# Kernel tuning notes

Measured on AMD Instinct MI355X. Metric: run time of the kernel, lower is better.

Reference implementation:

```python
import jax, jax.numpy as jnp
import numpy as np

B, T, D, H, F = 4, 2048, 1024, 16, 4096
HD = D // H
EPS = 1e-5


def setup_inputs() -> dict:
    key = jax.random.key(0)
    ks = jax.random.split(key, 10)
    s = lambda fan_in: 1.0 / np.sqrt(fan_in)
    return {
        "x": jax.random.normal(ks[0], (B, T, D), jnp.float32),
        "ln1_g": jnp.ones((D,), jnp.float32),
        "ln1_b": jnp.zeros((D,), jnp.float32),
        "ln2_g": jnp.ones((D,), jnp.float32),
        "ln2_b": jnp.zeros((D,), jnp.float32),
        "Wq": jax.random.normal(ks[1], (H, D, HD), jnp.float32) * s(D),
        "Wk": jax.random.normal(ks[2], (H, D, HD), jnp.float32) * s(D),
        "Wv": jax.random.normal(ks[3], (H, D, HD), jnp.float32) * s(D),
        "Wo": jax.random.normal(ks[4], (D, D), jnp.float32) * s(D),
        "bo": jnp.zeros((D,), jnp.float32),
        "W1": jax.random.normal(ks[5], (D, F), jnp.float32) * s(D),
        "b1": jnp.zeros((F,), jnp.float32),
        "W2": jax.random.normal(ks[6], (F, D), jnp.float32) * s(F),
        "b2": jnp.zeros((D,), jnp.float32),
    }


def _layernorm(x, g, b):
    mu = jnp.mean(x, axis=-1, keepdims=True)
    var = jnp.mean(jnp.square(x - mu), axis=-1, keepdims=True)
    return (x - mu) * jax.lax.rsqrt(var + EPS) * g + b


def reference(x, ln1_g, ln1_b, ln2_g, ln2_b, Wq, Wk, Wv, Wo, bo, W1, b1, W2, b2):
    Bc, Tc, Dc = x.shape
    xn = _layernorm(x, ln1_g, ln1_b)
    # per-head projections (source loops over heads; here batched over h)
    q = jnp.einsum('btd,hdk->bhtk', xn, Wq)
    k = jnp.einsum('btd,hdk->bhtk', xn, Wk)
    v = jnp.einsum('btd,hdk->bhtk', xn, Wv)
    scale = jnp.asarray(Dc, x.dtype) ** -0.5  # C**-0.5 with C = embedding_dim
    scores = jnp.einsum('bhtk,bhsk->bhts', q, k) * scale
    causal = jnp.tril(jnp.ones((Tc, Tc), bool))
    scores = jnp.where(causal, scores, -jnp.inf)
    attn = jax.nn.softmax(scores, axis=-1)
    out = jnp.einsum('bhts,bhsk->bhtk', attn, v)
    out = out.transpose(0, 2, 1, 3).reshape(Bc, Tc, Dc)  # concat heads
    attn_out = out @ Wo + bo
    h = attn_out + x  # residual 1
    hn = _layernorm(h, ln2_g, ln2_b)
    ff = jax.nn.relu(hn @ W1 + b1) @ W2 + b2
    return ff + h  # residual 2
```

## Files before the change

### kernel.cpp

```cpp
#include <hip/hip_runtime.h>
#include <hip/hip_bf16.h>

#define NB 4
#define NT 2048
#define ND 1024
#define NH 16
#define NHD 64
#define NF 4096
#define MTOK (NB*NT)

typedef float f32x4 __attribute__((ext_vector_type(4)));
typedef __bf16 bf16x8 __attribute__((ext_vector_type(8)));
typedef short s16x8 __attribute__((ext_vector_type(8)));
typedef unsigned short ushort_t;

__device__ inline ushort_t f2bf(float f) {
    unsigned int u = __builtin_bit_cast(unsigned int, f);
    unsigned int r = (u + 0x7FFFu + ((u >> 16) & 1u)) >> 16;
    return (ushort_t)r;
}

__device__ __forceinline__ void async_load16(const void* g, void* l) {
    __builtin_amdgcn_global_load_lds(
        (const __attribute__((address_space(1))) void*)g,
        (__attribute__((address_space(3))) void*)l, 16, 0, 0);
}

__device__ __forceinline__ unsigned int cvt_pk_bf16(float lo, float hi) {
    unsigned int r;
    asm("v_cvt_pk_bf16_f32 %0, %1, %2" : "=v"(r) : "v"(lo), "v"(hi));
    return r;
}

__device__ __forceinline__ float exp2_fast(float x) {
    float r;
    asm("v_exp_f32 %0, %1" : "=v"(r) : "v"(x));
    return r;
}

__global__ __launch_bounds__(256)
void transpose_to_bf16(const float* __restrict__ src, ushort_t* __restrict__ dst,
                       int R, int C) {
    __shared__ float tile[32][33];
    int c0 = blockIdx.x * 32, r0 = blockIdx.y * 32;
    #pragma unroll
    for (int i = 0; i < 32; i += 8)
        tile[threadIdx.y + i][threadIdx.x] =
            src[(size_t)(r0 + threadIdx.y + i) * C + c0 + threadIdx.x];
    __syncthreads();
    #pragma unroll
    for (int i = 0; i < 32; i += 8)
        dst[(size_t)(c0 + threadIdx.y + i) * R + r0 + threadIdx.x] =
            f2bf(tile[threadIdx.x][threadIdx.y + i]);
}

__global__ __launch_bounds__(256)
void transpose_qkv_to_bf16(const float* __restrict__ Wq, const float* __restrict__ Wk,
                           const float* __restrict__ Wv, ushort_t* __restrict__ dst) {
    __shared__ float tile[32][33];
    int z = blockIdx.z;
    int w = z >> 4, h = z & 15;
    const float* src = (w == 0 ? Wq : (w == 1 ? Wk : Wv)) + (size_t)h * ND * NHD;
    const float sc = (w == 0) ? 0.03125f * 1.44269504f : 1.0f;
    ushort_t* out = dst + ((size_t)w * ND + h * NHD) * ND;
    int c0 = blockIdx.x * 32, r0 = blockIdx.y * 32;
    #pragma unroll
    for (int i = 0; i < 32; i += 8)
        tile[threadIdx.y + i][threadIdx.x] =
            src[(size_t)(r0 + threadIdx.y + i) * NHD + c0 + threadIdx.x];
    __syncthreads();
    #pragma unroll
    for (int i = 0; i < 32; i += 8)
        out[(size_t)(c0 + threadIdx.y + i) * ND + r0 + threadIdx.x] =
            f2bf(tile[threadIdx.x][threadIdx.y + i] * sc);
}

__global__ __launch_bounds__(256)
void layernorm_to_bf16(const float* __restrict__ x, const float* __restrict__ g,
                       const float* __restrict__ bvec, ushort_t* __restrict__ out) {
    int row = blockIdx.x;
    const float4* xr = (const float4*)(x + (size_t)row * ND);
    float4 v = xr[threadIdx.x];
    float s = v.x + v.y + v.z + v.w;
    float s2 = v.x * v.x + v.y * v.y + v.z * v.z + v.w * v.w;
    #pragma unroll
    for (int o = 32; o >= 1; o >>= 1) {
        s += __shfl_xor(s, o);
        s2 += __shfl_xor(s2, o);
    }
    __shared__ float red[8];
    int wave = threadIdx.x >> 6, lane = threadIdx.x & 63;
    if (lane == 0) { red[wave] = s; red[4 + wave] = s2; }
    __syncthreads();
    float ts = red[0] + red[1] + red[2] + red[3];
    float ts2 = red[4] + red[5] + red[6] + red[7];
    float mu = ts * (1.f / ND);
    float var = ts2 * (1.f / ND) - mu * mu;
    float rs = rsqrtf(var + 1e-5f);
    float4 gv = ((const float4*)g)[threadIdx.x];
    float4 bv = ((const float4*)bvec)[threadIdx.x];
    ushort4 o4;
    o4.x = f2bf((v.x - mu) * rs * gv.x + bv.x);
    o4.y = f2bf((v.y - mu) * rs * gv.y + bv.y);
    o4.z = f2bf((v.z - mu) * rs * gv.z + bv.z);
    o4.w = f2bf((v.w - mu) * rs * gv.w + bv.w);
    ((ushort4*)(out + (size_t)row * ND))[threadIdx.x] = o4;
}

template<int BN, bool HAS_BIAS, bool RELU, bool HAS_RES, bool OUT_F32>
__global__ __launch_bounds__(512, 2)
void gemm256(const ushort_t* __restrict__ A, const ushort_t* __restrict__ Bt,
             const float* __restrict__ bias, const float* __restrict__ res,
             void* __restrict__ outp, int M, int N, int K) {
    constexpr int NFR = BN / 64;
    constexpr int BISS = BN / 64;
    __shared__ __align__(16) ushort_t As[2][256 * 64];
    __shared__ __align__(16) ushort_t Bs[2][BN * 64];
    const int t = threadIdx.x;
    const int wave = t >> 6, lane = t & 63;
    const int wm = wave >> 2, wn = wave & 3;
    const int g = lane >> 4, l16 = lane & 15;
    int wid = blockIdx.y * gridDim.x + blockIdx.x;
    const int cpx = (gridDim.x * gridDim.y) >> 3;
    wid = (wid & 7) * cpx + (wid >> 3);
    const int m0 = (wid / gridDim.x) * 256;
    const int n0 = (wid % gridDim.x) * BN;
    const int lrow8 = lane >> 3;
    const int srcCol = ((lane & 7) ^ lrow8) * 8;
    const ushort_t* Abase = A + (size_t)m0 * K + srcCol;
    const ushort_t* Bbase = Bt + (size_t)n0 * K + srcCol;
    const int NKT = K >> 6;

    f32x4 acc[8][NFR] = {};

    auto stageA = [&](int kt, int slot) {
        #pragma unroll
        for (int j = 0; j < 4; j++) {
            const int rowbase = j * 64 + wave * 8;
            async_load16(Abase + (size_t)(rowbase + lrow8) * K + kt * 64,
                         &As[slot][rowbase * 64]);
        }
    };
    auto stageB = [&](int kt, int slot) {
        #pragma unroll
        for (int j = 0; j < BISS; j++) {
            const int rowbase = j * 64 + wave * 8;
            async_load16(Bbase + (size_t)(rowbase + lrow8) * K + kt * 64,
                         &Bs[slot][rowbase * 64]);
        }
    };

    stageA(0, 0);
    stageB(0, 0);
    stageB(1, 1);

    for (int kt = 0; kt < NKT; ++kt) {
        const int cur = kt & 1;
        if (kt == NKT - 1) {
            asm volatile("s_waitcnt vmcnt(0)" ::: "memory");
        } else if constexpr (BN == 256) {
            asm volatile("s_waitcnt vmcnt(4)" ::: "memory");
        } else {
            asm volatile("s_waitcnt vmcnt(2)" ::: "memory");
        }
        __builtin_amdgcn_s_barrier();

        const ushort_t* as = As[cur];
        const ushort_t* bs = Bs[cur];

        bf16x8 bfr[NFR][2];
        #pragma unroll
        for (int nf = 0; nf < NFR; nf++)
            #pragma unroll
            for (int ks = 0; ks < 2; ks++) {
                const int row = wn * (BN / 4) + nf * 16 + l16;
                int a = row * 128 + ks * 64 + 16 * g;
                a ^= (row & 7) << 4;
                bfr[nf][ks] = *(const bf16x8*)((const char*)bs + a);
            }
        if (kt + 1 < NKT) stageA(kt + 1, cur ^ 1);

        #pragma unroll
        for (int q = 0; q < 4; q++) {
            if (q == 2) {
                __builtin_amdgcn_s_barrier();
                if (kt + 2 < NKT) stageB(kt + 2, cur);
            }
            bf16x8 af[2][2];
            #pragma unroll
            for (int mi2 = 0; mi2 < 2; mi2++)
                #pragma unroll
                for (int ks = 0; ks < 2; ks++) {
                    const int row = wm * 128 + (q * 2 + mi2) * 16 + l16;
                    int a = row * 128 + ks * 64 + 16 * g;
                    a ^= (row & 7) << 4;
                    af[mi2][ks] = *(const bf16x8*)((const char*)as + a);
                }
            __builtin_amdgcn_s_setprio(1);
            #pragma unroll
            for (int mi2 = 0; mi2 < 2; mi2++)
                #pragma unroll
                for (int nf = 0; nf < NFR; nf++)
                    #pragma unroll
                    for (int ks = 0; ks < 2; ks++)
                        acc[q * 2 + mi2][nf] = __builtin_amdgcn_mfma_f32_16x16x32_bf16(
                            af[mi2][ks], bfr[nf][ks], acc[q * 2 + mi2][nf], 0, 0, 0);
            __builtin_amdgcn_s_setprio(0);
        }
    }

    const int gr0 = m0 + wm * 128 + g * 4;
    const int gc0 = n0 + wn * (BN / 4) + l16;
    #pragma unroll
    for (int mi = 0; mi < 8; mi++) {
        #pragma unroll
        for (int nf = 0; nf < NFR; nf++) {
            const int col = gc0 + nf * 16;
            float bb = 0.f;
            if constexpr (HAS_BIAS) bb = bias[col];
            #pragma unroll
            for (int r = 0; r < 4; r++) {
                const int row = gr0 + mi * 16 + r;
                float v = acc[mi][nf][r] + bb;
                if constexpr (RELU) v = fmaxf(v, 0.f);
                if constexpr (HAS_RES) v += res[(size_t)row * N + col];
                if constexpr (OUT_F32)
                    ((float*)outp)[(size_t)row * N + col] = v;
                else
                    ((ushort_t*)outp)[(size_t)row * N + col] = f2bf(v);
            }
        }
    }
}

__global__ __launch_bounds__(256)
void attn_kernel(const ushort_t* __restrict__ qkv, ushort_t* __restrict__ out) {
    __shared__ __align__(16) ushort_t Ks[2][64 * 64];
    __shared__ __align__(16) ushort_t Vt[2][64 * 64];
    __shared__ unsigned int Pw[4][32][35];
    const int L = blockIdx.y * gridDim.x + blockIdx.x;
    const int xcd = L & 7, kk = L >> 3;
    const int bh = ((kk & 7) << 3) | xcd;
    const int pairIdx = kk >> 3;
    const int b = bh >> 4, h = bh & 15;
    const int t = threadIdx.x, wave = t >> 6, lane = t & 63;
    const int g = lane >> 4, q16 = lane & 15;
    const size_t base = ((size_t)b * NT) * 3072 + h * NHD;
    const ushort_t* qp_base = qkv + base;
    const ushort_t* kb = qkv + base + 1024;
    const ushort_t* vb = qkv + base + 2048;
    const int krw = lane >> 3, kck = lane & 7;
    const int ksrc = (kck ^ krw) * 8;
    const int vkp = t >> 3, vdg = t & 7;

    bf16x8 ones_f;
    {
        uint4 u = {0x3F803F80u, 0x3F803F80u, 0x3F803F80u, 0x3F803F80u};
        ones_f = __builtin_bit_cast(bf16x8, u);
    }

    auto stageK = [&](int kv, int buf) {
        #pragma unroll
        for (int c = 0; c < 2; c++) {
            const int rowbase = c * 32 + wave * 8;
            async_load16(kb + (size_t)(kv * 64 + rowbase + krw) * 3072 + ksrc,
                         &Ks[buf][rowbase * 64]);
        }
    };
    auto loadV = [&](int kv, s16x8& v0, s16x8& v1) {
        const ushort_t* vp = vb + (size_t)(kv * 64 + 2 * vkp) * 3072 + vdg * 8;
        v0 = *(const s16x8*)vp;
        v1 = *(const s16x8*)(vp + 3072);
    };
    auto writeV = [&](int buf, const s16x8& v0, const s16x8& v1) {
        const uint4 w0 = __builtin_bit_cast(uint4, v0);
        const uint4 w1 = __builtin_bit_cast(uint4, v1);
        const unsigned int lw0[4] = {w0.x, w0.y, w0.z, w0.w};
        const unsigned int lw1[4] = {w1.x, w1.y, w1.z, w1.w};
        #pragma unroll
        for (int j = 0; j < 4; j++) {
            unsigned int we = __builtin_amdgcn_perm(lw1[j], lw0[j], 0x05040100u);
            unsigned int wo = __builtin_amdgcn_perm(lw1[j], lw0[j], 0x07060302u);
            int d0 = vdg * 8 + 2 * j;
            int a0 = (d0 << 7) + (vkp << 2);
            a0 ^= ((((d0) & 7) ^ (((d0) >> 3) & 7)) << 4);
            *(unsigned int*)((char*)&Vt[buf][0] + a0) = we;
            int d1 = d0 + 1;
            int a1 = (d1 << 7) + (vkp << 2);
            a1 ^= ((((d1) & 7) ^ (((d1) >> 3) & 7)) << 4);
            *(unsigned int*)((char*)&Vt[buf][0] + a1) = wo;
        }
    };

    for (int half = 0; half < 2; half++) {
        const int qt = half ? (15 - pairIdx) : pairIdx;
        const int q0 = qt * 128;
        const int wq0 = q0 + wave * 32;
        bf16x8 qf[2][2];
        #pragma unroll
        for (int qb2 = 0; qb2 < 2; qb2++) {
            const ushort_t* qp = qp_base + (size_t)(wq0 + 16 * qb2 + q16) * 3072 + 8 * g;
            qf[qb2][0] = *(const bf16x8*)qp;
            qf[qb2][1] = *(const bf16x8*)(qp + 32);
        }
        f32x4 of[2][4] = {};
        f32x4 of4[2] = {};
        const int nkv = 2 * qt + 2;

        {
            s16x8 pv0, pv1;
            stageK(0, 0);
            loadV(0, pv0, pv1);
            asm volatile("s_waitcnt vmcnt(0)" ::: "memory");
            writeV(0, pv0, pv1);
        }
        __syncthreads();

        for (int kv = 0; kv < nkv; ++kv) {
            const int cur = kv & 1, nxt = cur ^ 1;
            s16x8 pv0, pv1;
            const bool pre = (kv + 1 < nkv);
            if (pre) {
                stageK(kv + 1, nxt);
                loadV(kv + 1, pv0, pv1);
            }
            __builtin_amdgcn_sched_barrier(0);

            const int kbase = kv * 64;
            if (kbase <= wq0 + 31) {
                bf16x8 kf[4][2];
                #pragma unroll
                for (int n = 0; n < 4; n++)
                    #pragma unroll
                    for (int kd = 0; kd < 2; kd++) {
                        int row = n * 16 + q16;
                        int a = row * 128 + (kd * 64 + 16 * g);
                        a ^= ((row & 7) << 4);
                        kf[n][kd] = *(const bf16x8*)((const char*)&Ks[cur][0] + a);
                    }

                f32x4 sf[2][4] = {};
                #pragma unroll
                for (int n = 0; n < 4; n++)
                    #pragma unroll
                    for (int kd = 0; kd < 2; kd++) {
                        sf[0][n] = __builtin_amdgcn_mfma_f32_16x16x32_bf16(
                            kf[n][kd], qf[0][kd], sf[0][n], 0, 0, 0);
                        sf[1][n] = __builtin_amdgcn_mfma_f32_16x16x32_bf16(
                            kf[n][kd], qf[1][kd], sf[1][n], 0, 0, 0);
                    }

                #pragma unroll
                for (int qb2 = 0; qb2 < 2; qb2++) {
                    const int wqb = wq0 + 16 * qb2 + q16;
                    const bool partial = (kbase + 63 > wq0 + 16 * qb2);
                    float p[4][4];
                    #pragma unroll
                    for (int n = 0; n < 4; n++)
                        #pragma unroll
                        for (int r = 0; r < 4; r++) {
                            float v = sf[qb2][n][r];
                            if (partial) {
                                int kg = kbase + n * 16 + 4 * g + r;
                                if (kg > wqb) v = -1.0e30f;
                            }
                            p[n][r] = exp2_fast(v);
                        }
                    unsigned int* pr = &Pw[wave][16 * qb2 + q16][0];
                    #pragma unroll
                    for (int n = 0; n < 4; n++) {
                        pr[8 * n + 2 * g + 0] = cvt_pk_bf16(p[n][0], p[n][1]);
                        pr[8 * n + 2 * g + 1] = cvt_pk_bf16(p[n][2], p[n][3]);
                    }
                }

                #pragma unroll
                for (int kbk = 0; kbk < 2; kbk++) {
                    bf16x8 pfr[2];
                    #pragma unroll
                    for (int qb2 = 0; qb2 < 2; qb2++) {
                        const unsigned int* pr = &Pw[wave][16 * qb2 + q16][0];
                        uint4 pu;
                        pu.x = pr[16 * kbk + 4 * g + 0];
                        pu.y = pr[16 * kbk + 4 * g + 1];
                        pu.z = pr[16 * kbk + 4 * g + 2];
                        pu.w = pr[16 * kbk + 4 * g + 3];
                        pfr[qb2] = __builtin_bit_cast(bf16x8, pu);
                    }
                    of4[0] = __builtin_amdgcn_mfma_f32_16x16x32_bf16(
                        ones_f, pfr[0], of4[0], 0, 0, 0);
                    of4[1] = __builtin_amdgcn_mfma_f32_16x16x32_bf16(
                        ones_f, pfr[1], of4[1], 0, 0, 0);
                    #pragma unroll
                    for (int nf = 0; nf < 4; nf++) {
                        const int d = nf * 16 + q16;
                        int a = (d << 7) + (kbk * 64 + 16 * g);
                        a ^= (((d & 7) ^ ((d >> 3) & 7)) << 4);
                        bf16x8 vf = *(const bf16x8*)((const char*)&Vt[cur][0] + a);
                        of[0][nf] = __builtin_amdgcn_mfma_f32_16x16x32_bf16(
                            vf, pfr[0], of[0][nf], 0, 0, 0);
                        of[1][nf] = __builtin_amdgcn_mfma_f32_16x16x32_bf16(
                            vf, pfr[1], of[1][nf], 0, 0, 0);
                    }
                }
            }

            if (pre) writeV(nxt, pv0, pv1);
            __syncthreads();
        }

        #pragma unroll
        for (int qb2 = 0; qb2 < 2; qb2++) {
            float rl = 1.f / of4[qb2][0];
            const size_t orow = (size_t)b * NT + q0 + wave * 32 + 16 * qb2 + q16;
            #pragma unroll
            for (int nf = 0; nf < 4; nf++) {
                ushort4 o4;
                o4.x = f2bf(of[qb2][nf][0] * rl);
                o4.y = f2bf(of[qb2][nf][1] * rl);
                o4.z = f2bf(of[qb2][nf][2] * rl);
                o4.w = f2bf(of[qb2][nf][3] * rl);
                *(ushort4*)(out + orow * ND + h * NHD + nf * 16 + 4 * g) = o4;
            }
        }
    }
}

extern "C" void kernel_launch(void* const* d_in, const int* in_sizes, int n_in,
                              void* d_out, int out_size, void* d_ws, size_t ws_size,
                              hipStream_t stream) {
    const float* x     = (const float*)d_in[0];
    const float* ln1_g = (const float*)d_in[1];
    const float* ln1_b = (const float*)d_in[2];
    const float* ln2_g = (const float*)d_in[3];
    const float* ln2_b = (const float*)d_in[4];
    const float* Wq    = (const float*)d_in[5];
    const float* Wk    = (const float*)d_in[6];
    const float* Wv    = (const float*)d_in[7];
    const float* Wo    = (const float*)d_in[8];
    const float* bo    = (const float*)d_in[9];
    const float* W1    = (const float*)d_in[10];
    const float* b1    = (const float*)d_in[11];
    const float* W2    = (const float*)d_in[12];
    const float* b2    = (const float*)d_in[13];
    float* outp = (float*)d_out;

    char* w = (char*)d_ws;
    ushort_t* Wqkv_t = (ushort_t*)(w);
    ushort_t* Wo_t   = (ushort_t*)(w + 6291456);
    ushort_t* W1_t   = (ushort_t*)(w + 8388608);
    ushort_t* W2_t   = (ushort_t*)(w + 16777216);
    ushort_t* xn     = (ushort_t*)(w + 25165824);
    ushort_t* qkv    = (ushort_t*)(w + 41943040);
    ushort_t* attn_o = qkv + (size_t)MTOK * 3072;
    ushort_t* ff1    = qkv;
    float*    hbuf   = (float*)(w + 41943040 + 67108864);

    dim3 tb(32, 8);
    transpose_qkv_to_bf16<<<dim3(2, 32, 48), tb, 0, stream>>>(Wq, Wk, Wv, Wqkv_t);
    transpose_to_bf16<<<dim3(32, 32), tb, 0, stream>>>(Wo, Wo_t, 1024, 1024);
    transpose_to_bf16<<<dim3(128, 32), tb, 0, stream>>>(W1, W1_t, 1024, 4096);
    transpose_to_bf16<<<dim3(32, 128), tb, 0, stream>>>(W2, W2_t, 4096, 1024);

    layernorm_to_bf16<<<MTOK, 256, 0, stream>>>(x, ln1_g, ln1_b, xn);

    gemm256<128, false, false, false, false><<<dim3(24, 32), 512, 0, stream>>>(
        xn, Wqkv_t, nullptr, nullptr, qkv, MTOK, 3072, 1024);

    attn_kernel<<<dim3(8, 64), 256, 0, stream>>>(qkv, attn_o);

    gemm256<128, true, false, true, true><<<dim3(8, 32), 512, 0, stream>>>(
        attn_o, Wo_t, bo, x, hbuf, MTOK, 1024, 1024);

    layernorm_to_bf16<<<MTOK, 256, 0, stream>>>(hbuf, ln2_g, ln2_b, xn);

    gemm256<256, true, true, false, false><<<dim3(16, 32), 512, 0, stream>>>(
        xn, W1_t, b1, nullptr, ff1, MTOK, NF, 1024);

    gemm256<128, true, false, true, true><<<dim3(8, 32), 512, 0, stream>>>(
        ff1, W2_t, b2, hbuf, outp, MTOK, 1024, NF);
}
```

Measured before the change: 379.1 us.

## Restructure GEMM into 8-phase pipelined loads and store residual h in bf16

Reworks the GEMM main loop so that global-to-LDS loads for A and B are split into halves and issued across four quarter-phases, with barriers and sched_barriers around each MFMA block. The row mapping of waves changes to interleave in 64-row chunks. This is meant to spread memory traffic evenly and overlap it with compute. Separately, the intermediate residual h is now stored as bf16 instead of fp32, with a new bf16-input layernorm and a bf16 residual mode in the final GEMM. That cuts memory traffic but loses precision in the residual path and adds extra barriers per iteration.

```diff
diff --git a/kernel.cpp b/kernel.cpp
--- a/kernel.cpp
+++ b/kernel.cpp
@@ -18,6 +18,9 @@
     unsigned int u = __builtin_bit_cast(unsigned int, f);
     unsigned int r = (u + 0x7FFFu + ((u >> 16) & 1u)) >> 16;
     return (ushort_t)r;
+}
+__device__ inline float bf2f(ushort_t u) {
+    return __builtin_bit_cast(float, (unsigned int)u << 16);
 }
 
 __device__ __forceinline__ void async_load16(const void* g, void* l) {
@@ -107,13 +110,45 @@
     ((ushort4*)(out + (size_t)row * ND))[threadIdx.x] = o4;
 }
 
-template<int BN, bool HAS_BIAS, bool RELU, bool HAS_RES, bool OUT_F32>
+__global__ __launch_bounds__(256)
+void layernorm_bf16(const ushort_t* __restrict__ x, const float* __restrict__ g,
+                    const float* __restrict__ bvec, ushort_t* __restrict__ out) {
+    int row = blockIdx.x;
+    ushort4 u4 = ((const ushort4*)(x + (size_t)row * ND))[threadIdx.x];
+    float4 v;
+    v.x = bf2f(u4.x); v.y = bf2f(u4.y); v.z = bf2f(u4.z); v.w = bf2f(u4.w);
+    float s = v.x + v.y + v.z + v.w;
+    float s2 = v.x * v.x + v.y * v.y + v.z * v.z + v.w * v.w;
+    #pragma unroll
+    for (int o = 32; o >= 1; o >>= 1) {
+        s += __shfl_xor(s, o);
+        s2 += __shfl_xor(s2, o);
+    }
+    __shared__ float red[8];
+    int wave = threadIdx.x >> 6, lane = threadIdx.x & 63;
+    if (lane == 0) { red[wave] = s; red[4 + wave] = s2; }
+    __syncthreads();
+    float ts = red[0] + red[1] + red[2] + red[3];
+    float ts2 = red[4] + red[5] + red[6] + red[7];
+    float mu = ts * (1.f / ND);
+    float var = ts2 * (1.f / ND) - mu * mu;
+    float rs = rsqrtf(var + 1e-5f);
+    float4 gv = ((const float4*)g)[threadIdx.x];
+    float4 bv = ((const float4*)bvec)[threadIdx.x];
+    ushort4 o4;
+    o4.x = f2bf((v.x - mu) * rs * gv.x + bv.x);
+    o4.y = f2bf((v.y - mu) * rs * gv.y + bv.y);
+    o4.z = f2bf((v.z - mu) * rs * gv.z + bv.z);
+    o4.w = f2bf((v.w - mu) * rs * gv.w + bv.w);
+    ((ushort4*)(out + (size_t)row * ND))[threadIdx.x] = o4;
+}
+
+template<int BN, bool HAS_BIAS, bool RELU, int RES_MODE, bool OUT_F32>
 __global__ __launch_bounds__(512, 2)
-void gemm256(const ushort_t* __restrict__ A, const ushort_t* __restrict__ Bt,
-             const float* __restrict__ bias, const float* __restrict__ res,
-             void* __restrict__ outp, int M, int N, int K) {
+void gemm8p(const ushort_t* __restrict__ A, const ushort_t* __restrict__ Bt,
+            const float* __restrict__ bias, const void* __restrict__ res,
+            void* __restrict__ outp, int M, int N, int K) {
     constexpr int NFR = BN / 64;
-    constexpr int BISS = BN / 64;
     __shared__ __align__(16) ushort_t As[2][256 * 64];
     __shared__ __align__(16) ushort_t Bs[2][BN * 64];
     const int t = threadIdx.x;
@@ -133,69 +168,82 @@
 
     f32x4 acc[8][NFR] = {};
 
-    auto stageA = [&](int kt, int slot) {
-        #pragma unroll
-        for (int j = 0; j < 4; j++) {
+    auto stageAhalf = [&](int kt, int h, int slot) {
+        #pragma unroll
+        for (int j = 2 * h; j < 2 * h + 2; j++) {
             const int rowbase = j * 64 + wave * 8;
             async_load16(Abase + (size_t)(rowbase + lrow8) * K + kt * 64,
                          &As[slot][rowbase * 64]);
         }
     };
-    auto stageB = [&](int kt, int slot) {
-        #pragma unroll
-        for (int j = 0; j < BISS; j++) {
-            const int rowbase = j * 64 + wave * 8;
+    auto stageBhalf = [&](int kt, int h, int slot) {
+        if constexpr (BN == 256) {
+            #pragma unroll
+            for (int j = 2 * h; j < 2 * h + 2; j++) {
+                const int rowbase = j * 64 + wave * 8;
+                async_load16(Bbase + (size_t)(rowbase + lrow8) * K + kt * 64,
+                             &Bs[slot][rowbase * 64]);
+            }
+        } else {
+            const int rowbase = h * 64 + wave * 8;
             async_load16(Bbase + (size_t)(rowbase + lrow8) * K + kt * 64,
                          &Bs[slot][rowbase * 64]);
         }
     };
 
-    stageA(0, 0);
-    stageB(0, 0);
-    stageB(1, 1);
+    stageAhalf(0, 0, 0); stageAhalf(0, 1, 0);
+    stageBhalf(0, 0, 0); stageBhalf(0, 1, 0);
+    stageBhalf(1, 0, 1); stageBhalf(1, 1, 1);
+    stageAhalf(1, 0, 1);
+    if constexpr (BN == 256) asm volatile("s_waitcnt vmcnt(6)" ::: "memory");
+    else                     asm volatile("s_waitcnt vmcnt(4)" ::: "memory");
+    __builtin_amdgcn_s_barrier();
+    __builtin_amdgcn_sched_barrier(0);
 
     for (int kt = 0; kt < NKT; ++kt) {
-        const int cur = kt & 1;
-        if (kt == NKT - 1) {
-            asm volatile("s_waitcnt vmcnt(0)" ::: "memory");
-        } else if constexpr (BN == 256) {
-            asm volatile("s_waitcnt vmcnt(4)" ::: "memory");
-        } else {
-            asm volatile("s_waitcnt vmcnt(2)" ::: "memory");
-        }
-        __builtin_amdgcn_s_barrier();
-
+        const int cur = kt & 1, nxt = cur ^ 1;
         const ushort_t* as = As[cur];
         const ushort_t* bs = Bs[cur];
-
         bf16x8 bfr[NFR][2];
         #pragma unroll
-        for (int nf = 0; nf < NFR; nf++)
-            #pragma unroll
-            for (int ks = 0; ks < 2; ks++) {
-                const int row = wn * (BN / 4) + nf * 16 + l16;
-                int a = row * 128 + ks * 64 + 16 * g;
-                a ^= (row & 7) << 4;
-                bfr[nf][ks] = *(const bf16x8*)((const char*)bs + a);
-            }
-        if (kt + 1 < NKT) stageA(kt + 1, cur ^ 1);
-
-        #pragma unroll
         for (int q = 0; q < 4; q++) {
-            if (q == 2) {
-                __builtin_amdgcn_s_barrier();
-                if (kt + 2 < NKT) stageB(kt + 2, cur);
+            if (q == 0) {
+                #pragma unroll
+                for (int nf = 0; nf < NFR; nf++)
+                    #pragma unroll
+                    for (int ks = 0; ks < 2; ks++) {
+                        const int row = wn * (BN / 4) + nf * 16 + l16;
+                        int a = row * 128 + ks * 64 + 16 * g;
+                        a ^= (row & 7) << 4;
+                        bfr[nf][ks] = *(const bf16x8*)((const char*)bs + a);
+                    }
             }
             bf16x8 af[2][2];
             #pragma unroll
             for (int mi2 = 0; mi2 < 2; mi2++)
                 #pragma unroll
                 for (int ks = 0; ks < 2; ks++) {
-                    const int row = wm * 128 + (q * 2 + mi2) * 16 + l16;
+                    const int row = q * 64 + wm * 32 + mi2 * 16 + l16;
                     int a = row * 128 + ks * 64 + 16 * g;
                     a ^= (row & 7) << 4;
                     af[mi2][ks] = *(const bf16x8*)((const char*)as + a);
                 }
+            if (q == 0)      { if (kt + 1 < NKT) stageAhalf(kt + 1, 1, nxt); }
+            else if (q == 1) { if (kt + 2 < NKT) stageBhalf(kt + 2, 0, cur); }
+            else if (q == 2) { if (kt + 2 < NKT) stageBhalf(kt + 2, 1, cur); }
+            else             { if (kt + 2 < NKT) stageAhalf(kt + 2, 0, cur); }
+            __builtin_amdgcn_sched_barrier(0);
+            if (q == 3) {
+                if (kt >= NKT - 2) {
+                    asm volatile("s_waitcnt vmcnt(0)" ::: "memory");
+                } else if constexpr (BN == 256) {
+                    asm volatile("s_waitcnt vmcnt(6)" ::: "memory");
+                } else {
+                    asm volatile("s_waitcnt vmcnt(4)" ::: "memory");
+                }
+            }
+            __builtin_amdgcn_s_barrier();
+            __builtin_amdgcn_sched_barrier(0);
             __builtin_amdgcn_s_setprio(1);
             #pragma unroll
             for (int mi2 = 0; mi2 < 2; mi2++)
@@ -206,13 +254,15 @@
                         acc[q * 2 + mi2][nf] = __builtin_amdgcn_mfma_f32_16x16x32_bf16(
                             af[mi2][ks], bfr[nf][ks], acc[q * 2 + mi2][nf], 0, 0, 0);
             __builtin_amdgcn_s_setprio(0);
+            __builtin_amdgcn_s_barrier();
+            __builtin_amdgcn_sched_barrier(0);
         }
     }
 
-    const int gr0 = m0 + wm * 128 + g * 4;
     const int gc0 = n0 + wn * (BN / 4) + l16;
     #pragma unroll
     for (int mi = 0; mi < 8; mi++) {
+        const int rowb = m0 + (mi >> 1) * 64 + wm * 32 + (mi & 1) * 16 + g * 4;
         #pragma unroll
         for (int nf = 0; nf < NFR; nf++) {
             const int col = gc0 + nf * 16;
@@ -220,10 +270,13 @@
             if constexpr (HAS_BIAS) bb = bias[col];
             #pragma unroll
             for (int r = 0; r < 4; r++) {
-                const int row = gr0 + mi * 16 + r;
+                const int row = rowb + r;
                 float v = acc[mi][nf][r] + bb;
                 if constexpr (RELU) v = fmaxf(v, 0.f);
-                if constexpr (HAS_RES) v += res[(size_t)row * N + col];
+                if constexpr (RES_MODE == 1)
+                    v += ((const float*)res)[(size_t)row * N + col];
+                else if constexpr (RES_MODE == 2)
+                    v += bf2f(((const ushort_t*)res)[(size_t)row * N + col]);
                 if constexpr (OUT_F32)
                     ((float*)outp)[(size_t)row * N + col] = v;
                 else
@@ -454,7 +507,7 @@
     ushort_t* qkv    = (ushort_t*)(w + 41943040);
     ushort_t* attn_o = qkv + (size_t)MTOK * 3072;
     ushort_t* ff1    = qkv;
-    float*    hbuf   = (float*)(w + 41943040 + 67108864);
+    ushort_t* hbuf   = (ushort_t*)(w + 41943040 + 67108864);
 
     dim3 tb(32, 8);
     transpose_qkv_to_bf16<<<dim3(2, 32, 48), tb, 0, stream>>>(Wq, Wk, Wv, Wqkv_t);
@@ -464,19 +517,19 @@
 
     layernorm_to_bf16<<<MTOK, 256, 0, stream>>>(x, ln1_g, ln1_b, xn);
 
-    gemm256<128, false, false, false, false><<<dim3(24, 32), 512, 0, stream>>>(
+    gemm8p<128, false, false, 0, false><<<dim3(24, 32), 512, 0, stream>>>(
         xn, Wqkv_t, nullptr, nullptr, qkv, MTOK, 3072, 1024);
 
     attn_kernel<<<dim3(8, 64), 256, 0, stream>>>(qkv, attn_o);
 
-    gemm256<128, true, false, true, true><<<dim3(8, 32), 512, 0, stream>>>(
+    gemm8p<128, true, false, 1, false><<<dim3(8, 32), 512, 0, stream>>>(
         attn_o, Wo_t, bo, x, hbuf, MTOK, 1024, 1024);
 
-    layernorm_to_bf16<<<MTOK, 256, 0, stream>>>(hbuf, ln2_g, ln2_b, xn);
-
-    gemm256<256, true, true, false, false><<<dim3(16, 32), 512, 0, stream>>>(
+    layernorm_bf16<<<MTOK, 256, 0, stream>>>(hbuf, ln2_g, ln2_b, xn);
+
+    gemm8p<256, true, true, 0, false><<<dim3(16, 32), 512, 0, stream>>>(
         xn, W1_t, b1, nullptr, ff1, MTOK, NF, 1024);
 
-    gemm256<128, true, false, true, true><<<dim3(8, 32), 512, 0, stream>>>(
+    gemm8p<128, true, false, 2, true><<<dim3(8, 32), 512, 0, stream>>>(
         ff1, W2_t, b2, hbuf, outp, MTOK, 1024, NF);
 }
```

After: 378.1 us. Within noise of the previous version (-0.3%).
